# Kernel tuning notes

Measured on AMD Instinct MI355X. Metric: run time of the kernel, lower is better.

The kernel has to match this reference:

```python
import jax, jax.numpy as jnp
import numpy as np

N = 100000   # nodes
E = 220000   # directed edges (each branch)
H = 128      # hidden_dim
OUT = 1      # output_dim
G = 4096     # num graphs in batch
PE = 5       # laplacian eigenvector PE dims
VOCAB = 28   # atom types


def gcn_conv(x, src, dst, W, b, n):
    # PyG GCNConv: x' = D^-1/2 (A + I) D^-1/2 (X W) + b
    h = x @ W
    deg = jax.ops.segment_sum(jnp.ones(src.shape[0], x.dtype), dst, num_segments=n) + 1.0
    dinv = jax.lax.rsqrt(deg)
    coef = dinv[src] * dinv[dst]                                    # [E]
    agg = jax.ops.segment_sum(h[src] * coef[:, None], dst, num_segments=n)
    agg = agg + h * (dinv * dinv)[:, None]                          # self-loop term
    return agg + b


def gcn2(x, edge_index, W1, b1, W2, b2, n):
    # PyG GCN model, num_layers=2: conv -> relu -> conv
    src, dst = edge_index[0], edge_index[1]
    h = jax.nn.relu(gcn_conv(x, src, dst, W1, b1, n))
    return gcn_conv(h, src, dst, W2, b2, n)


def setup_inputs() -> dict:
    key = jax.random.key(0)
    ks = jax.random.split(key, 16)
    s = 0.1
    return {
        "node_tokens": jax.random.randint(ks[0], (N, 1), 0, VOCAB),
        "pe": jax.random.normal(ks[1], (N, PE), jnp.float32),
        "edge_index": jax.random.randint(ks[2], (2, E), 0, N),
        "vr_edge_index": jax.random.randint(ks[3], (2, E), 0, N),
        "batch": jnp.sort(jax.random.randint(ks[4], (N,), 0, G)),
        "embed_table": jax.random.normal(ks[5], (VOCAB, H), jnp.float32) * s,
        "Wt": jax.random.normal(ks[6], (PE, H), jnp.float32) * s,
        "bt": jnp.zeros((H,), jnp.float32),
        "W1": jax.random.normal(ks[7], (H, H), jnp.float32) * s,
        "b1": jnp.zeros((H,), jnp.float32),
        "W2": jax.random.normal(ks[8], (H, OUT), jnp.float32) * s,
        "b2": jnp.zeros((OUT,), jnp.float32),
        "Wv1": jax.random.normal(ks[9], (H, H), jnp.float32) * s,
        "bv1": jnp.zeros((H,), jnp.float32),
        "Wv2": jax.random.normal(ks[10], (H, OUT), jnp.float32) * s,
        "bv2": jnp.zeros((OUT,), jnp.float32),
    }


def reference(node_tokens, pe, edge_index, vr_edge_index, batch, embed_table,
              Wt, bt, W1, b1, W2, b2, Wv1, bv1, Wv2, bv2):
    # embed_x(data.x.long()).squeeze(1) + lin_trans(pe)
    x = embed_table[node_tokens[:, 0]] + (pe @ Wt + bt)             # [N, H]
    x1 = gcn2(x, edge_index, W1, b1, W2, b2, N)                     # [N, OUT]
    xv = gcn2(x, vr_edge_index, Wv1, bv1, Wv2, bv2, N)              # [N, OUT]
    x1 = x1 + xv
    y_hat = jax.ops.segment_sum(x1, batch, num_segments=G)          # [G, OUT]
    y_hat = jnp.squeeze(y_hat, axis=-1)                             # [G]
    return (y_hat, x)
```

## Files before the change

kernel.cpp:

```cpp
#include <hip/hip_runtime.h>

#define NN 100000
#define NE 220000
#define HD 128
#define NG 4096
#define NPE 5
#define NB_SCAN ((NN + 255) / 256)
#define NBX4 ((NN * HD / 4) / 256)
#define NT16 (NN / 16)
#define NBGEMM 1024
#define NBW 128
#define NBZ ((2 * NN + 255) / 256)
#define NBE2 14
#define NBD ((2 * NE + 255) / 256)

typedef unsigned int uint;
typedef unsigned short ushort;
typedef __attribute__((ext_vector_type(8))) short bf16x8;
typedef __attribute__((ext_vector_type(4))) float f32x4;

__device__ __forceinline__ float bf2f(uint u16) {
    return __uint_as_float(u16 << 16);
}
__device__ __forceinline__ ushort f2bf(float f) {
    uint u = __float_as_uint(f);
    u += 0x7fffu + ((u >> 16) & 1u);
    return (ushort)(u >> 16);
}

__global__ void k_prep0(const float* __restrict__ W1, const float* __restrict__ Wv1,
                        const float* __restrict__ embed, const float* __restrict__ bt,
                        ushort* __restrict__ Wcat, int* __restrict__ cnt,
                        float* __restrict__ embed2) {
    int b = blockIdx.x;
    if (b < NBW) {
        int t = b * 256 + threadIdx.x;
        int f = t >> 7, k = t & 127;
        const float* W = (f < HD) ? W1 : Wv1;
        Wcat[t] = f2bf(W[k * HD + (f & 127)]);
    } else if (b < NBW + NBZ) {
        int t = (b - NBW) * 256 + threadIdx.x;
        if (t < 2 * NN) cnt[t] = 0;
    } else {
        int t = (b - NBW - NBZ) * 256 + threadIdx.x;
        if (t < 28 * 128) embed2[t] = embed[t] + bt[t & 127];
    }
}

__global__ void k_front(const int* __restrict__ tok, const float* __restrict__ pe,
                        const float* __restrict__ embed2, const float* __restrict__ Wtr,
                        float* __restrict__ x, ushort* __restrict__ xb,
                        const int* __restrict__ ei, const int* __restrict__ vei,
                        int* __restrict__ cnt) {
    int b = blockIdx.x;
    if (b < NBX4) {
        int idx = b * 256 + threadIdx.x;
        int n = idx >> 5, q = idx & 31;
        int t = tok[n];
        float4 acc = ((const float4*)(embed2 + (size_t)t * HD))[q];
        const float* pen = pe + n * NPE;
#pragma unroll
        for (int k = 0; k < NPE; ++k) {
            float p = pen[k];
            float4 wv = ((const float4*)(Wtr + k * HD))[q];
            acc.x += p * wv.x; acc.y += p * wv.y;
            acc.z += p * wv.z; acc.w += p * wv.w;
        }
        ((float4*)x)[idx] = acc;
        uint2 pk;
        pk.x = (uint)f2bf(acc.x) | ((uint)f2bf(acc.y) << 16);
        pk.y = (uint)f2bf(acc.z) | ((uint)f2bf(acc.w) << 16);
        ((uint2*)xb)[idx] = pk;
    } else {
        int t = (b - NBX4) * 256 + threadIdx.x;
        if (t < 2 * NE) {
            int br = t >= NE;
            int e = t - br * NE;
            const int* S = br ? vei : ei;
            atomicAdd(&cnt[br * NN + S[NE + e]], 1);
        }
    }
}

__global__ __launch_bounds__(256) void k_gemm(const ushort* __restrict__ xb,
                                              const ushort* __restrict__ Wt,
                                              ushort* __restrict__ H) {
    int w = threadIdx.x >> 6;
    int lane = threadIdx.x & 63;
    int m = lane & 15, quad = lane >> 4;
    const ushort* Wbase = Wt + ((size_t)(w * 4) * 16 + m) * 128 + quad * 8;
    bf16x8 wf[4][4];
#pragma unroll
    for (int j = 0; j < 4; ++j)
#pragma unroll
        for (int kc = 0; kc < 4; ++kc)
            wf[j][kc] = *(const bf16x8*)(Wbase + (size_t)j * 16 * 128 + kc * 32);

    for (int t = blockIdx.x; t < NT16; t += NBGEMM) {
        int n = t * 16 + m;
        const ushort* Arow = xb + (size_t)n * HD + quad * 8;
        bf16x8 xf[4];
#pragma unroll
        for (int kc = 0; kc < 4; ++kc)
            xf[kc] = *(const bf16x8*)(Arow + kc * 32);
        f32x4 acc[4] = {};
#pragma unroll
        for (int j = 0; j < 4; ++j)
#pragma unroll
            for (int kc = 0; kc < 4; ++kc)
                acc[j] = __builtin_amdgcn_mfma_f32_16x16x32_bf16(wf[j][kc], xf[kc],
                                                                 acc[j], 0, 0, 0);
#pragma unroll
        for (int j = 0; j < 4; ++j) {
            f32x4 a = acc[j];
            uint2 pk;
            pk.x = (uint)f2bf(a[0]) | ((uint)f2bf(a[1]) << 16);
            pk.y = (uint)f2bf(a[2]) | ((uint)f2bf(a[3]) << 16);
            *(uint2*)&H[(size_t)n * 256 + (w * 4 + j) * 16 + quad * 4] = pk;
        }
    }
}

__global__ void k_scan1(const int* __restrict__ cnt, int* __restrict__ off,
                        int* __restrict__ bsum, float* __restrict__ dinv,
                        float* __restrict__ y) {
    __shared__ int s[256];
    int tid = threadIdx.x;
    int gid = blockIdx.x * 256 + tid;
    if (gid < NG) y[gid] = 0.f;
    int br = blockIdx.x / NB_SCAN;
    int blk = blockIdx.x % NB_SCAN;
    int i = blk * 256 + tid;
    int v = (i < NN) ? cnt[br * NN + i] : 0;
    if (i < NN) dinv[br * NN + i] = rsqrtf((float)v + 1.0f);
    s[tid] = v;
    __syncthreads();
    for (int d = 1; d < 256; d <<= 1) {
        int t = (tid >= d) ? s[tid - d] : 0;
        __syncthreads();
        s[tid] += t;
        __syncthreads();
    }
    if (i < NN) off[br * NN + i] = s[tid] - v;
    if (tid == 255) bsum[br * 512 + blk] = s[255];
}

__global__ void k_scan3(const int* __restrict__ off, const int* __restrict__ bsum,
                        const int* __restrict__ cnt, int2* __restrict__ off2,
                        int* __restrict__ cur) {
    __shared__ int s[256];
    int br = blockIdx.x / NB_SCAN;
    int blk = blockIdx.x % NB_SCAN;
    int tid = threadIdx.x;
    int v = 0;
    if (tid < blk) v = bsum[br * 512 + tid];
    if (tid + 256 < blk) v += bsum[br * 512 + tid + 256];
    s[tid] = v;
#pragma unroll
    for (int d = 128; d > 0; d >>= 1) {
        __syncthreads();
        if (tid < d) s[tid] += s[tid + d];
    }
    __syncthreads();
    int pre = s[0];
    int i = blk * 256 + tid;
    if (i < NN) {
        int o = off[br * NN + i] + pre;
        int2 pr;
        pr.x = o;
        pr.y = o + cnt[br * NN + i];
        off2[br * NN + i] = pr;
        cur[br * NN + i] = o;
    }
}

__global__ void k_scatter(const int* __restrict__ ei, const int* __restrict__ vei,
                          const float* __restrict__ dinv, int* __restrict__ cur,
                          int2* __restrict__ ent) {
    int t = blockIdx.x * blockDim.x + threadIdx.x;
    if (t >= 2 * NE) return;
    int br = t >= NE;
    int e = t - br * NE;
    const int* S = br ? vei : ei;
    int s = S[e], d = S[NE + e];
    int pos = atomicAdd(&cur[br * NN + d], 1);
    int2 rec;
    rec.x = s;
    rec.y = __float_as_int(dinv[br * NN + s] * dinv[br * NN + d]);
    ent[br * NE + pos] = rec;
}

__global__ void k_gather_ep(const ushort* __restrict__ H, const float* __restrict__ dinv,
                            const int2* __restrict__ off2,
                            const int2* __restrict__ ent,
                            const float* __restrict__ b1, const float* __restrict__ bv1,
                            const float* __restrict__ W2, const float* __restrict__ Wv2,
                            float* __restrict__ z) {
    int wid = threadIdx.x >> 6;
    int lane = threadIdx.x & 63;
    int half = lane >> 5;
    int l = lane & 31;
    int task = blockIdx.x * 8 + wid * 2 + half;
    int br = task >= NN;
    int n = task - br * NN;

    const int2* en = ent + br * NE;
    size_t hoff = (size_t)br * 128;

    float dv = dinv[br * NN + n];
    uint2 u = *(const uint2*)(H + (size_t)n * 256 + hoff + l * 4);
    float c = dv * dv;
    float a0 = bf2f(u.x & 0xffffu) * c, a1 = bf2f(u.x >> 16) * c;
    float a2 = bf2f(u.y & 0xffffu) * c, a3 = bf2f(u.y >> 16) * c;

    int2 pr = off2[br * NN + n];
    int p0 = pr.x, p1 = pr.y;
    for (int p = p0; p < p1; p += 4) {
        int2 e0 = en[p], e1 = en[p + 1], e2 = en[p + 2], e3 = en[p + 3];
        int s0 = e0.x;
        int s1 = (p + 1 < p1) ? e1.x : n;
        int s2 = (p + 2 < p1) ? e2.x : n;
        int s3 = (p + 3 < p1) ? e3.x : n;
        float c0 = __int_as_float(e0.y);
        float c1 = (p + 1 < p1) ? __int_as_float(e1.y) : 0.f;
        float c2 = (p + 2 < p1) ? __int_as_float(e2.y) : 0.f;
        float c3 = (p + 3 < p1) ? __int_as_float(e3.y) : 0.f;
        uint2 v0 = *(const uint2*)(H + (size_t)s0 * 256 + hoff + l * 4);
        uint2 v1 = *(const uint2*)(H + (size_t)s1 * 256 + hoff + l * 4);
        uint2 v2 = *(const uint2*)(H + (size_t)s2 * 256 + hoff + l * 4);
        uint2 v3 = *(const uint2*)(H + (size_t)s3 * 256 + hoff + l * 4);
        a0 += bf2f(v0.x & 0xffffu) * c0; a1 += bf2f(v0.x >> 16) * c0;
        a2 += bf2f(v0.y & 0xffffu) * c0; a3 += bf2f(v0.y >> 16) * c0;
        a0 += bf2f(v1.x & 0xffffu) * c1; a1 += bf2f(v1.x >> 16) * c1;
        a2 += bf2f(v1.y & 0xffffu) * c1; a3 += bf2f(v1.y >> 16) * c1;
        a0 += bf2f(v2.x & 0xffffu) * c2; a1 += bf2f(v2.x >> 16) * c2;
        a2 += bf2f(v2.y & 0xffffu) * c2; a3 += bf2f(v2.y >> 16) * c2;
        a0 += bf2f(v3.x & 0xffffu) * c3; a1 += bf2f(v3.x >> 16) * c3;
        a2 += bf2f(v3.y & 0xffffu) * c3; a3 += bf2f(v3.y >> 16) * c3;
    }

    const float* bb = br ? bv1 : b1;
    const float* ww = br ? Wv2 : W2;
    float4 b4 = *(const float4*)&bb[l * 4];
    float4 w4 = *(const float4*)&ww[l * 4];
    float part = fmaxf(a0 + b4.x, 0.f) * w4.x + fmaxf(a1 + b4.y, 0.f) * w4.y
               + fmaxf(a2 + b4.z, 0.f) * w4.z + fmaxf(a3 + b4.w, 0.f) * w4.w;
#pragma unroll
    for (int o = 16; o > 0; o >>= 1) part += __shfl_down(part, o, 32);
    if (l == 0) z[br * NN + n] = part;
}

__global__ void k_final2(const float* __restrict__ z, const float* __restrict__ dinv,
                         const int2* __restrict__ off2,
                         const int2* __restrict__ ent,
                         const float* __restrict__ b2, const float* __restrict__ bv2,
                         const int* __restrict__ batch, float* __restrict__ y) {
    __shared__ float ybuf[256];
    __shared__ int gbase_s;
    int br = blockIdx.x >= NB_SCAN;
    int nb = blockIdx.x - br * NB_SCAN;
    int tid = threadIdx.x;
    ybuf[tid] = 0.f;
    if (tid == 0) gbase_s = batch[nb * 256];
    __syncthreads();
    int gbase = gbase_s;
    int n = nb * 256 + tid;
    if (n < NN) {
        const int2* en = ent + br * NE;
        float dv = dinv[br * NN + n];
        float acc = z[br * NN + n] * dv * dv;
        int2 pr = off2[br * NN + n];
        int p1 = pr.y;
        for (int p = pr.x; p < p1; p += 4) {
            int2 e0 = en[p], e1 = en[p + 1], e2 = en[p + 2], e3 = en[p + 3];
            int s0 = e0.x;
            int s1 = (p + 1 < p1) ? e1.x : n;
            int s2 = (p + 2 < p1) ? e2.x : n;
            int s3 = (p + 3 < p1) ? e3.x : n;
            float c0 = __int_as_float(e0.y);
            float c1 = (p + 1 < p1) ? __int_as_float(e1.y) : 0.f;
            float c2 = (p + 2 < p1) ? __int_as_float(e2.y) : 0.f;
            float c3 = (p + 3 < p1) ? __int_as_float(e3.y) : 0.f;
            acc += c0 * z[br * NN + s0] + c1 * z[br * NN + s1]
                 + c2 * z[br * NN + s2] + c3 * z[br * NN + s3];
        }
        acc += br ? bv2[0] : b2[0];
        int gi = batch[n] - gbase;
        if (gi < 256) atomicAdd(&ybuf[gi], acc);
        else atomicAdd(&y[batch[n]], acc);
    }
    __syncthreads();
    float v = ybuf[tid];
    if (v != 0.f) atomicAdd(&y[gbase + tid], v);
}

extern "C" void kernel_launch(void* const* d_in, const int* in_sizes, int n_in,
                              void* d_out, int out_size, void* d_ws, size_t ws_size,
                              hipStream_t stream) {
    const int*   tok   = (const int*)d_in[0];
    const float* pe    = (const float*)d_in[1];
    const int*   ei    = (const int*)d_in[2];
    const int*   vei   = (const int*)d_in[3];
    const int*   batch = (const int*)d_in[4];
    const float* embed = (const float*)d_in[5];
    const float* Wtr   = (const float*)d_in[6];
    const float* bt    = (const float*)d_in[7];
    const float* W1    = (const float*)d_in[8];
    const float* b1    = (const float*)d_in[9];
    const float* W2    = (const float*)d_in[10];
    const float* b2    = (const float*)d_in[11];
    const float* Wv1   = (const float*)d_in[12];
    const float* bv1   = (const float*)d_in[13];
    const float* Wv2   = (const float*)d_in[14];
    const float* bv2   = (const float*)d_in[15];

    float* y = (float*)d_out;
    float* x = y + NG;

    char* w = (char*)d_ws;
    ushort* xb   = (ushort*)w;               w += (size_t)NN * HD * 2;
    ushort* H    = (ushort*)w;               w += (size_t)NN * 256 * 2;
    ushort* Wcat = (ushort*)w;               w += 256 * 128 * 2;
    float*  emb2 = (float*)w;                w += 28 * 128 * 4;
    float*  dinv = (float*)w;                w += 2 * NN * 4;
    float*  z    = (float*)w;                w += 2 * NN * 4;
    int*    cnt  = (int*)w;                  w += 2 * NN * 4;
    int*    off  = (int*)w;                  w += 2 * NN * 4;
    int*    cur  = (int*)w;                  w += 2 * NN * 4;
    int2*   off2 = (int2*)w;                 w += (size_t)2 * NN * 8;
    int2*   ent  = (int2*)w;                 w += (size_t)(2 * NE + 8) * 8;
    int*    bsum = (int*)w;                  w += 2 * 512 * 4;

    k_prep0<<<NBW + NBZ + NBE2, 256, 0, stream>>>(W1, Wv1, embed, bt, Wcat, cnt, emb2);
    k_front<<<NBX4 + NBD, 256, 0, stream>>>(tok, pe, emb2, Wtr, x, xb, ei, vei, cnt);
    k_gemm<<<NBGEMM, 256, 0, stream>>>(xb, Wcat, H);
    k_scan1<<<2 * NB_SCAN, 256, 0, stream>>>(cnt, off, bsum, dinv, y);
    k_scan3<<<2 * NB_SCAN, 256, 0, stream>>>(off, bsum, cnt, off2, cur);
    k_scatter<<<NBD, 256, 0, stream>>>(ei, vei, dinv, cur, ent);
    k_gather_ep<<<2 * NN / 8, 256, 0, stream>>>(H, dinv, off2, ent,
                                                b1, bv1, W2, Wv2, z);
    k_final2<<<2 * NB_SCAN, 256, 0, stream>>>(z, dinv, off2, ent,
                                              b2, bv2, batch, y);
}
```

Baseline: 231.7 us.

## Fuse GEMM with scan1 and reuse count-atomic ranks for CSR scatter

The value returned by the degree-count atomic is now stored as a per-edge rank, so the scatter kernel computes positions as offset plus rank instead of running a second atomic pass over a cursor array. The separate GEMM and first scan kernels are merged into one launch whose leading blocks do the scan and whose remaining blocks do the MFMA GEMM, removing a kernel boundary. In exchange it writes and reads an extra per-edge rank array, and the ordering of edges within each row stays nondeterministic.

```diff
diff --git a/kernel.cpp b/kernel.cpp
--- a/kernel.cpp
+++ b/kernel.cpp
@@ -51,7 +51,7 @@
                         const float* __restrict__ embed2, const float* __restrict__ Wtr,
                         float* __restrict__ x, ushort* __restrict__ xb,
                         const int* __restrict__ ei, const int* __restrict__ vei,
-                        int* __restrict__ cnt) {
+                        int* __restrict__ cnt, int* __restrict__ rank) {
     int b = blockIdx.x;
     if (b < NBX4) {
         int idx = b * 256 + threadIdx.x;
@@ -77,77 +77,77 @@
             int br = t >= NE;
             int e = t - br * NE;
             const int* S = br ? vei : ei;
-            atomicAdd(&cnt[br * NN + S[NE + e]], 1);
-        }
-    }
-}
-
-__global__ __launch_bounds__(256) void k_gemm(const ushort* __restrict__ xb,
-                                              const ushort* __restrict__ Wt,
-                                              ushort* __restrict__ H) {
-    int w = threadIdx.x >> 6;
-    int lane = threadIdx.x & 63;
-    int m = lane & 15, quad = lane >> 4;
-    const ushort* Wbase = Wt + ((size_t)(w * 4) * 16 + m) * 128 + quad * 8;
-    bf16x8 wf[4][4];
-#pragma unroll
-    for (int j = 0; j < 4; ++j)
-#pragma unroll
-        for (int kc = 0; kc < 4; ++kc)
-            wf[j][kc] = *(const bf16x8*)(Wbase + (size_t)j * 16 * 128 + kc * 32);
-
-    for (int t = blockIdx.x; t < NT16; t += NBGEMM) {
-        int n = t * 16 + m;
-        const ushort* Arow = xb + (size_t)n * HD + quad * 8;
-        bf16x8 xf[4];
-#pragma unroll
-        for (int kc = 0; kc < 4; ++kc)
-            xf[kc] = *(const bf16x8*)(Arow + kc * 32);
-        f32x4 acc[4] = {};
+            rank[t] = atomicAdd(&cnt[br * NN + S[NE + e]], 1);
+        }
+    }
+}
+
+__global__ __launch_bounds__(256) void k_gemm_scan1(
+        const ushort* __restrict__ xb, const ushort* __restrict__ Wt,
+        ushort* __restrict__ H,
+        const int* __restrict__ cnt, int* __restrict__ off,
+        int* __restrict__ bsum, float* __restrict__ dinv, float* __restrict__ y) {
+    __shared__ int s[256];
+    int b = blockIdx.x;
+    if (b < 2 * NB_SCAN) {
+        int tid = threadIdx.x;
+        int gid = b * 256 + tid;
+        if (gid < NG) y[gid] = 0.f;
+        int br = b / NB_SCAN;
+        int blk = b % NB_SCAN;
+        int i = blk * 256 + tid;
+        int v = (i < NN) ? cnt[br * NN + i] : 0;
+        if (i < NN) dinv[br * NN + i] = rsqrtf((float)v + 1.0f);
+        s[tid] = v;
+        __syncthreads();
+        for (int d = 1; d < 256; d <<= 1) {
+            int t = (tid >= d) ? s[tid - d] : 0;
+            __syncthreads();
+            s[tid] += t;
+            __syncthreads();
+        }
+        if (i < NN) off[br * NN + i] = s[tid] - v;
+        if (tid == 255) bsum[br * 512 + blk] = s[255];
+    } else {
+        int w = threadIdx.x >> 6;
+        int lane = threadIdx.x & 63;
+        int m = lane & 15, quad = lane >> 4;
+        const ushort* Wbase = Wt + ((size_t)(w * 4) * 16 + m) * 128 + quad * 8;
+        bf16x8 wf[4][4];
 #pragma unroll
         for (int j = 0; j < 4; ++j)
 #pragma unroll
             for (int kc = 0; kc < 4; ++kc)
-                acc[j] = __builtin_amdgcn_mfma_f32_16x16x32_bf16(wf[j][kc], xf[kc],
-                                                                 acc[j], 0, 0, 0);
-#pragma unroll
-        for (int j = 0; j < 4; ++j) {
-            f32x4 a = acc[j];
-            uint2 pk;
-            pk.x = (uint)f2bf(a[0]) | ((uint)f2bf(a[1]) << 16);
-            pk.y = (uint)f2bf(a[2]) | ((uint)f2bf(a[3]) << 16);
-            *(uint2*)&H[(size_t)n * 256 + (w * 4 + j) * 16 + quad * 4] = pk;
-        }
-    }
-}
-
-__global__ void k_scan1(const int* __restrict__ cnt, int* __restrict__ off,
-                        int* __restrict__ bsum, float* __restrict__ dinv,
-                        float* __restrict__ y) {
-    __shared__ int s[256];
-    int tid = threadIdx.x;
-    int gid = blockIdx.x * 256 + tid;
-    if (gid < NG) y[gid] = 0.f;
-    int br = blockIdx.x / NB_SCAN;
-    int blk = blockIdx.x % NB_SCAN;
-    int i = blk * 256 + tid;
-    int v = (i < NN) ? cnt[br * NN + i] : 0;
-    if (i < NN) dinv[br * NN + i] = rsqrtf((float)v + 1.0f);
-    s[tid] = v;
-    __syncthreads();
-    for (int d = 1; d < 256; d <<= 1) {
-        int t = (tid >= d) ? s[tid - d] : 0;
-        __syncthreads();
-        s[tid] += t;
-        __syncthreads();
-    }
-    if (i < NN) off[br * NN + i] = s[tid] - v;
-    if (tid == 255) bsum[br * 512 + blk] = s[255];
+                wf[j][kc] = *(const bf16x8*)(Wbase + (size_t)j * 16 * 128 + kc * 32);
+
+        for (int t = b - 2 * NB_SCAN; t < NT16; t += NBGEMM) {
+            int n = t * 16 + m;
+            const ushort* Arow = xb + (size_t)n * HD + quad * 8;
+            bf16x8 xf[4];
+#pragma unroll
+            for (int kc = 0; kc < 4; ++kc)
+                xf[kc] = *(const bf16x8*)(Arow + kc * 32);
+            f32x4 acc[4] = {};
+#pragma unroll
+            for (int j = 0; j < 4; ++j)
+#pragma unroll
+                for (int kc = 0; kc < 4; ++kc)
+                    acc[j] = __builtin_amdgcn_mfma_f32_16x16x32_bf16(wf[j][kc], xf[kc],
+                                                                     acc[j], 0, 0, 0);
+#pragma unroll
+            for (int j = 0; j < 4; ++j) {
+                f32x4 a = acc[j];
+                uint2 pk;
+                pk.x = (uint)f2bf(a[0]) | ((uint)f2bf(a[1]) << 16);
+                pk.y = (uint)f2bf(a[2]) | ((uint)f2bf(a[3]) << 16);
+                *(uint2*)&H[(size_t)n * 256 + (w * 4 + j) * 16 + quad * 4] = pk;
+            }
+        }
+    }
 }
 
 __global__ void k_scan3(const int* __restrict__ off, const int* __restrict__ bsum,
-                        const int* __restrict__ cnt, int2* __restrict__ off2,
-                        int* __restrict__ cur) {
+                        const int* __restrict__ cnt, int2* __restrict__ off2) {
     __shared__ int s[256];
     int br = blockIdx.x / NB_SCAN;
     int blk = blockIdx.x % NB_SCAN;
@@ -170,20 +170,19 @@
         pr.x = o;
         pr.y = o + cnt[br * NN + i];
         off2[br * NN + i] = pr;
-        cur[br * NN + i] = o;
     }
 }
 
 __global__ void k_scatter(const int* __restrict__ ei, const int* __restrict__ vei,
-                          const float* __restrict__ dinv, int* __restrict__ cur,
-                          int2* __restrict__ ent) {
+                          const int* __restrict__ rank, const float* __restrict__ dinv,
+                          const int2* __restrict__ off2, int2* __restrict__ ent) {
     int t = blockIdx.x * blockDim.x + threadIdx.x;
     if (t >= 2 * NE) return;
     int br = t >= NE;
     int e = t - br * NE;
     const int* S = br ? vei : ei;
     int s = S[e], d = S[NE + e];
-    int pos = atomicAdd(&cur[br * NN + d], 1);
+    int pos = off2[br * NN + d].x + rank[t];
     int2 rec;
     rec.x = s;
     rec.y = __float_as_int(dinv[br * NN + s] * dinv[br * NN + d]);
@@ -207,14 +206,15 @@
     const int2* en = ent + br * NE;
     size_t hoff = (size_t)br * 128;
 
+    int2 pr = off2[br * NN + n];
+    int p0 = pr.x, p1 = pr.y;
+
     float dv = dinv[br * NN + n];
     uint2 u = *(const uint2*)(H + (size_t)n * 256 + hoff + l * 4);
     float c = dv * dv;
     float a0 = bf2f(u.x & 0xffffu) * c, a1 = bf2f(u.x >> 16) * c;
     float a2 = bf2f(u.y & 0xffffu) * c, a3 = bf2f(u.y >> 16) * c;
 
-    int2 pr = off2[br * NN + n];
-    int p0 = pr.x, p1 = pr.y;
     for (int p = p0; p < p1; p += 4) {
         int2 e0 = en[p], e1 = en[p + 1], e2 = en[p + 2], e3 = en[p + 3];
         int s0 = e0.x;
@@ -326,17 +326,18 @@
     float*  z    = (float*)w;                w += 2 * NN * 4;
     int*    cnt  = (int*)w;                  w += 2 * NN * 4;
     int*    off  = (int*)w;                  w += 2 * NN * 4;
-    int*    cur  = (int*)w;                  w += 2 * NN * 4;
+    int*    rank = (int*)w;                  w += (size_t)2 * NE * 4;
     int2*   off2 = (int2*)w;                 w += (size_t)2 * NN * 8;
     int2*   ent  = (int2*)w;                 w += (size_t)(2 * NE + 8) * 8;
     int*    bsum = (int*)w;                  w += 2 * 512 * 4;
 
     k_prep0<<<NBW + NBZ + NBE2, 256, 0, stream>>>(W1, Wv1, embed, bt, Wcat, cnt, emb2);
-    k_front<<<NBX4 + NBD, 256, 0, stream>>>(tok, pe, emb2, Wtr, x, xb, ei, vei, cnt);
-    k_gemm<<<NBGEMM, 256, 0, stream>>>(xb, Wcat, H);
-    k_scan1<<<2 * NB_SCAN, 256, 0, stream>>>(cnt, off, bsum, dinv, y);
-    k_scan3<<<2 * NB_SCAN, 256, 0, stream>>>(off, bsum, cnt, off2, cur);
-    k_scatter<<<NBD, 256, 0, stream>>>(ei, vei, dinv, cur, ent);
+    k_front<<<NBX4 + NBD, 256, 0, stream>>>(tok, pe, emb2, Wtr, x, xb, ei, vei,
+                                            cnt, rank);
+    k_gemm_scan1<<<2 * NB_SCAN + NBGEMM, 256, 0, stream>>>(xb, Wcat, H,
+                                                           cnt, off, bsum, dinv, y);
+    k_scan3<<<2 * NB_SCAN, 256, 0, stream>>>(off, bsum, cnt, off2);
+    k_scatter<<<NBD, 256, 0, stream>>>(ei, vei, rank, dinv, off2, ent);
     k_gather_ep<<<2 * NN / 8, 256, 0, stream>>>(H, dinv, off2, ent,
                                                 b1, bv1, W2, Wv2, z);
     k_final2<<<2 * NB_SCAN, 256, 0, stream>>>(z, dinv, off2, ent,
```

New measurement: 223.0 us. 1.04x faster.
